# Optimization experiments

Measured on AMD Instinct MI355X. Metric: run time of the kernel, lower is better.

The kernel has to match this reference:

```python
import jax, jax.numpy as jnp
import numpy as np

N_NODES = 75000
N_EDGES = 1200000


def gcn_conv(x, src, dst, W, b, n):
    # linear transform first (PyG GCNConv applies lin before propagate)
    h = x @ W  # [n, out]
    # add self loops
    loop = jnp.arange(n, dtype=src.dtype)
    s = jnp.concatenate([src, loop])
    d = jnp.concatenate([dst, loop])
    # symmetric normalization: deg computed on destination after self-loops
    deg = jnp.zeros((n,), dtype=h.dtype).at[d].add(1.0)
    dinv = jnp.where(deg > 0, jax.lax.rsqrt(deg), 0.0)
    norm = dinv[s] * dinv[d]  # [E+n]
    msgs = h[s] * norm[:, None]  # gather + scale, [E+n, out]
    out = jax.ops.segment_sum(msgs, d, num_segments=n)  # scatter-add
    return out + b


def setup_inputs() -> dict:
    key = jax.random.key(0)
    ks = jax.random.split(key, 6)
    x = jax.random.normal(ks[0], (N_NODES, 64), dtype=jnp.float32)
    edge_index = jax.random.randint(ks[1], (2, N_EDGES), 0, N_NODES, dtype=jnp.int64)
    # Glorot-ish scaled weights
    W1 = jax.random.normal(ks[2], (64, 64), dtype=jnp.float32) * (1.0 / np.sqrt(64))
    b1 = jax.random.normal(ks[3], (64,), dtype=jnp.float32) * 0.01
    W2 = jax.random.normal(ks[4], (64, 16), dtype=jnp.float32) * (1.0 / np.sqrt(64))
    b2 = jax.random.normal(ks[5], (16,), dtype=jnp.float32) * 0.01
    return {"x": x, "edge_index": edge_index, "W1": W1, "b1": b1, "W2": W2, "b2": b2}


def reference(x, edge_index, W1, b1, W2, b2):
    src, dst = edge_index[0], edge_index[1]
    h = gcn_conv(x, src, dst, W1, b1, N_NODES)
    h = jax.nn.relu(h)
    # dropout is identity in eval mode
    out = gcn_conv(h, src, dst, W2, b2, N_NODES)
    return out
```

## Files before the change

### kernel.cpp

```cpp
#include <hip/hip_runtime.h>


#define NBSHIFT 9
#define BUCKET_NODES 512
#define CAP 10240
#define CHA 8192
#define TA 512
#define TB 512
#define MAXNB 160
#define EPT 16

__device__ __forceinline__ unsigned bfpack(float a, float b) {
  unsigned ua = __float_as_uint(a), ub = __float_as_uint(b);
  ua += 0x7fffu + ((ua >> 16) & 1u);
  ub += 0x7fffu + ((ub >> 16) & 1u);
  return (ua >> 16) | (ub & 0xffff0000u);
}

__launch_bounds__(TA)
__global__ void kA_bucket(const int* __restrict__ src, const int* __restrict__ dst,
                          int* __restrict__ bucketCur, int* __restrict__ bucketArr,
                          int NB, int E) {
  __shared__ int stage[CHA];
  __shared__ unsigned char binOf[CHA];
  __shared__ int cnt[MAXNB];
  __shared__ int off[MAXNB];
  __shared__ int gpos[MAXNB];
  __shared__ int cursor[MAXNB];
  __shared__ int scanbuf[256];
  int t = threadIdx.x;
  int e0 = blockIdx.x * CHA;

  for (int i = t; i < NB; i += TA) cnt[i] = 0;
  __syncthreads();
  int dreg[EPT];
  #pragma unroll
  for (int j = 0; j < EPT; j++) {
    int e = e0 + t + j * TA;
    dreg[j] = (e < E) ? dst[e] : -1;
    if (dreg[j] >= 0) atomicAdd(&cnt[dreg[j] >> NBSHIFT], 1);
  }
  __syncthreads();
  if (t < 256) scanbuf[t] = (t < NB) ? cnt[t] : 0;
  __syncthreads();
  for (int o = 1; o < 256; o <<= 1) {
    int add = (t < 256 && t >= o) ? scanbuf[t - o] : 0;
    __syncthreads();
    if (t < 256) scanbuf[t] += add;
    __syncthreads();
  }
  if (t < NB) {
    off[t] = scanbuf[t] - cnt[t];
    cursor[t] = off[t];
    gpos[t] = (cnt[t] > 0) ? atomicAdd(&bucketCur[t], cnt[t]) : 0;
  }
  __syncthreads();
  #pragma unroll
  for (int j = 0; j < EPT; j++) {
    int e = e0 + t + j * TA;
    if (dreg[j] >= 0) {
      int d = dreg[j], s = src[e];
      int b = d >> NBSHIFT;
      int p = atomicAdd(&cursor[b], 1);
      stage[p] = (s << NBSHIFT) | (d & (BUCKET_NODES - 1));
      binOf[p] = (unsigned char)b;
    }
  }
  __syncthreads();
  int total = scanbuf[255];
  for (int i = t; i < total; i += TA) {
    int b = binOf[i];
    int destIdx = gpos[b] + (i - off[b]);
    if (destIdx < CAP) bucketArr[b * CAP + destIdx] = stage[i];
  }
}

__launch_bounds__(TB)
__global__ void kB_fill(const int* __restrict__ bucketArr, const int* __restrict__ bucketCur,
                        int* __restrict__ rp, float* __restrict__ dinv,
                        int* __restrict__ col, int N, int NB) {
  __shared__ int cnts[MAXNB];
  __shared__ int hist[BUCKET_NODES];
  __shared__ int cur[BUCKET_NODES];
  __shared__ int wsum[8], woff[8];
  __shared__ int s_base;
  int b = blockIdx.x;
  int t = threadIdx.x;
  int nE = min(bucketCur[b], CAP);
  int base = b * CAP;

  if (t < NB) cnts[t] = min(bucketCur[t], CAP);
  hist[t] = 0;
  __syncthreads();
  for (int i = t; i < nE; i += TB)
    atomicAdd(&hist[bucketArr[base + i] & (BUCKET_NODES - 1)], 1);
  __syncthreads();
  int myv = hist[t];
  int lane = t & 63, w = t >> 6;
  int incl = myv;
  #pragma unroll
  for (int o = 1; o < 64; o <<= 1) {
    int v = __shfl_up(incl, o);
    if (lane >= o) incl += v;
  }
  if (lane == 63) wsum[w] = incl;
  __syncthreads();
  if (t == 0) {
    int acc = 0;
    for (int i = 0; i < b; i++) acc += cnts[i];
    s_base = acc;
    int a2 = 0;
    #pragma unroll
    for (int i = 0; i < 8; i++) { woff[i] = a2; a2 += wsum[i]; }
    if (b == NB - 1) rp[N] = acc + nE;
  }
  __syncthreads();
  int gexcl = s_base + woff[w] + (incl - myv);
  cur[t] = gexcl;
  int gnode = b * BUCKET_NODES + t;
  if (gnode < N) {
    rp[gnode] = gexcl;
    dinv[gnode] = rsqrtf((float)(myv + 1));
  }
  __syncthreads();
  for (int i = t; i < nE; i += TB) {
    int v = bucketArr[base + i];
    int p = atomicAdd(&cur[v & (BUCKET_NODES - 1)], 1);
    col[p] = v >> NBSHIFT;
  }
}

__launch_bounds__(256)
__global__ void k_gemm64(const float4* __restrict__ X4, const float4* __restrict__ W4,
                         const float* __restrict__ dinv, uint2* __restrict__ outb,
                         int n) {
  __shared__ float4 Xs[64 * 17];
  __shared__ float4 Ws[64 * 16];
  int t = threadIdx.x;
  int base = blockIdx.x * 64;
  {
    int rr = t >> 2, q = t & 3;
    int r = base + rr;
    #pragma unroll
    for (int c = 0; c < 4; c++) {
      float4 v = make_float4(0.f, 0.f, 0.f, 0.f);
      if (r < n) v = X4[r * 16 + q * 4 + c];
      Xs[rr * 17 + q * 4 + c] = v;
      Ws[t + 256 * c] = W4[t + 256 * c];
    }
  }
  __syncthreads();

  int tx = t & 15, ty = t >> 4;
  float4 a0 = make_float4(0.f, 0.f, 0.f, 0.f), a1 = a0, a2 = a0, a3 = a0;
  #pragma unroll
  for (int kb = 0; kb < 16; kb++) {
    float4 x0 = Xs[(ty * 4 + 0) * 17 + kb];
    float4 x1 = Xs[(ty * 4 + 1) * 17 + kb];
    float4 x2 = Xs[(ty * 4 + 2) * 17 + kb];
    float4 x3 = Xs[(ty * 4 + 3) * 17 + kb];
    float4 w0 = Ws[(kb * 4 + 0) * 16 + tx];
    float4 w1 = Ws[(kb * 4 + 1) * 16 + tx];
    float4 w2 = Ws[(kb * 4 + 2) * 16 + tx];
    float4 w3 = Ws[(kb * 4 + 3) * 16 + tx];
    #define FMA4(A, XS) \
      A.x = fmaf(XS.x, w0.x, A.x); A.y = fmaf(XS.x, w0.y, A.y); \
      A.z = fmaf(XS.x, w0.z, A.z); A.w = fmaf(XS.x, w0.w, A.w); \
      A.x = fmaf(XS.y, w1.x, A.x); A.y = fmaf(XS.y, w1.y, A.y); \
      A.z = fmaf(XS.y, w1.z, A.z); A.w = fmaf(XS.y, w1.w, A.w); \
      A.x = fmaf(XS.z, w2.x, A.x); A.y = fmaf(XS.z, w2.y, A.y); \
      A.z = fmaf(XS.z, w2.z, A.z); A.w = fmaf(XS.z, w2.w, A.w); \
      A.x = fmaf(XS.w, w3.x, A.x); A.y = fmaf(XS.w, w3.y, A.y); \
      A.z = fmaf(XS.w, w3.z, A.z); A.w = fmaf(XS.w, w3.w, A.w);
    FMA4(a0, x0) FMA4(a1, x1) FMA4(a2, x2) FMA4(a3, x3)
    #undef FMA4
  }
  #pragma unroll
  for (int i = 0; i < 4; i++) {
    int r = base + ty * 4 + i;
    if (r < n) {
      float s = dinv[r];
      float4 a = (i == 0) ? a0 : (i == 1) ? a1 : (i == 2) ? a2 : a3;
      uint2 pk;
      pk.x = bfpack(a.x * s, a.y * s);
      pk.y = bfpack(a.z * s, a.w * s);
      outb[r * 16 + tx] = pk;
    }
  }
}

__launch_bounds__(256)
__global__ void k_agg64_w2(const uint2* __restrict__ hsb,
                           const int* __restrict__ rp,
                           const int* __restrict__ col,
                           const float* __restrict__ dinv,
                           const float* __restrict__ b1,
                           const float* __restrict__ W2,
                           unsigned* __restrict__ hs2b,
                           int n) {
  int lane = threadIdx.x & 63;
  int c = lane & 15;
  int sub = lane >> 4;
  int node = (blockIdx.x * blockDim.x + threadIdx.x) >> 6;
  if (node >= n) return;

  float4 b14 = ((const float4*)b1)[c];
  float w2r[16];
  #pragma unroll
  for (int i = 0; i < 16; i++) w2r[i] = W2[(sub * 16 + i) * 16 + c];

  int s0 = rp[node], s1 = rp[node + 1];
  int dt = s1 - s0 + 1;
  float ax = 0.f, ay = 0.f, az = 0.f, aw = 0.f;
  int t = sub;
  int i0 = 0, i1 = 0, i2 = 0, i3 = 0;
  if (t < dt)      i0 = (t == 0) ? node : col[s0 + t - 1];
  if (t + 4 < dt)  i1 = col[s0 + t + 3];
  if (t + 8 < dt)  i2 = col[s0 + t + 7];
  if (t + 12 < dt) i3 = col[s0 + t + 11];
  while (t < dt) {
    int c0 = i0, c1 = i1, c2 = i2, c3 = i3;
    bool h1 = (t + 4) < dt, h2 = (t + 8) < dt, h3 = (t + 12) < dt;
    int tn = t + 16;
    if (tn < dt)      i0 = col[s0 + tn - 1];
    if (tn + 4 < dt)  i1 = col[s0 + tn + 3];
    if (tn + 8 < dt)  i2 = col[s0 + tn + 7];
    if (tn + 12 < dt) i3 = col[s0 + tn + 11];
    uint2 u0 = hsb[c0 * 16 + c];
    uint2 u1 = h1 ? hsb[c1 * 16 + c] : make_uint2(0u, 0u);
    uint2 u2 = h2 ? hsb[c2 * 16 + c] : make_uint2(0u, 0u);
    uint2 u3 = h3 ? hsb[c3 * 16 + c] : make_uint2(0u, 0u);
    ax += __uint_as_float(u0.x << 16) + __uint_as_float(u1.x << 16)
        + __uint_as_float(u2.x << 16) + __uint_as_float(u3.x << 16);
    ay += __uint_as_float(u0.x & 0xffff0000u) + __uint_as_float(u1.x & 0xffff0000u)
        + __uint_as_float(u2.x & 0xffff0000u) + __uint_as_float(u3.x & 0xffff0000u);
    az += __uint_as_float(u0.y << 16) + __uint_as_float(u1.y << 16)
        + __uint_as_float(u2.y << 16) + __uint_as_float(u3.y << 16);
    aw += __uint_as_float(u0.y & 0xffff0000u) + __uint_as_float(u1.y & 0xffff0000u)
        + __uint_as_float(u2.y & 0xffff0000u) + __uint_as_float(u3.y & 0xffff0000u);
    t = tn;
  }
  #pragma unroll
  for (int m = 16; m <= 32; m <<= 1) {
    ax += __shfl_xor(ax, m);
    ay += __shfl_xor(ay, m);
    az += __shfl_xor(az, m);
    aw += __shfl_xor(aw, m);
  }
  float dv = dinv[node];
  float hx = fmaxf(ax * dv + b14.x, 0.f);
  float hy = fmaxf(ay * dv + b14.y, 0.f);
  float hz = fmaxf(az * dv + b14.z, 0.f);
  float hw = fmaxf(aw * dv + b14.w, 0.f);

  float part = 0.f;
  #pragma unroll
  for (int i = 0; i < 16; i++) {
    int srcLane = 4 * sub + (i >> 2);
    float h;
    if ((i & 3) == 0)      h = __shfl(hx, srcLane);
    else if ((i & 3) == 1) h = __shfl(hy, srcLane);
    else if ((i & 3) == 2) h = __shfl(hz, srcLane);
    else                   h = __shfl(hw, srcLane);
    part = fmaf(h, w2r[i], part);
  }
  #pragma unroll
  for (int m = 16; m <= 32; m <<= 1) part += __shfl_xor(part, m);
  part *= dv;
  float pnext = __shfl_down(part, 1);
  if (sub == 0 && (c & 1) == 0) {
    hs2b[node * 8 + (c >> 1)] = bfpack(part, pnext);
  }
}

__launch_bounds__(256)
__global__ void k_agg16(const uint2* __restrict__ hs2b,
                        const int* __restrict__ rp,
                        const int* __restrict__ col,
                        const float* __restrict__ dinv,
                        const float* __restrict__ b2,
                        float4* __restrict__ out4,
                        int n) {
  int lane = threadIdx.x & 63;
  int c = lane & 3;
  int sub = lane >> 2;
  int node = (blockIdx.x * blockDim.x + threadIdx.x) >> 6;
  if (node >= n) return;

  int s0 = rp[node], s1 = rp[node + 1];
  int dt = s1 - s0 + 1;
  float ax = 0.f, ay = 0.f, az = 0.f, aw = 0.f;
  int t = sub;
  int i0 = 0, i1 = 0;
  if (t < dt)      i0 = (t == 0) ? node : col[s0 + t - 1];
  if (t + 16 < dt) i1 = col[s0 + t + 15];
  while (t < dt) {
    int c0 = i0, c1 = i1;
    bool h1 = (t + 16) < dt;
    int tn = t + 32;
    if (tn < dt)      i0 = col[s0 + tn - 1];
    if (tn + 16 < dt) i1 = col[s0 + tn + 15];
    uint2 u0 = hs2b[c0 * 4 + c];
    uint2 u1 = h1 ? hs2b[c1 * 4 + c] : make_uint2(0u, 0u);
    ax += __uint_as_float(u0.x << 16) + __uint_as_float(u1.x << 16);
    ay += __uint_as_float(u0.x & 0xffff0000u) + __uint_as_float(u1.x & 0xffff0000u);
    az += __uint_as_float(u0.y << 16) + __uint_as_float(u1.y << 16);
    aw += __uint_as_float(u0.y & 0xffff0000u) + __uint_as_float(u1.y & 0xffff0000u);
    t = tn;
  }
  #pragma unroll
  for (int m = 4; m <= 32; m <<= 1) {
    ax += __shfl_xor(ax, m);
    ay += __shfl_xor(ay, m);
    az += __shfl_xor(az, m);
    aw += __shfl_xor(aw, m);
  }
  if (sub == 0) {
    float dv = dinv[node];
    float4 b24 = ((const float4*)b2)[c];
    float4 o;
    o.x = ax * dv + b24.x;
    o.y = ay * dv + b24.y;
    o.z = az * dv + b24.z;
    o.w = aw * dv + b24.w;
    out4[node * 4 + c] = o;
  }
}

extern "C" void kernel_launch(void* const* d_in, const int* in_sizes, int n_in,
                              void* d_out, int out_size, void* d_ws, size_t ws_size,
                              hipStream_t stream) {
  const float* x  = (const float*)d_in[0];
  const int* edges = (const int*)d_in[1];
  const float* W1 = (const float*)d_in[2];
  const float* b1 = (const float*)d_in[3];
  const float* W2 = (const float*)d_in[4];
  const float* b2 = (const float*)d_in[5];
  float* out = (float*)d_out;

  const int N = in_sizes[0] / 64;
  const int E = in_sizes[1] / 2;
  const int* src = edges;
  const int* dst = edges + E;
  const int NB = (N + BUCKET_NODES - 1) >> NBSHIFT;

  auto align = [](size_t v) { return (v + 255) & ~(size_t)255; };
  char* p = (char*)d_ws;
  float* dinv       = (float*)p; p += align((size_t)N * 4);
  int*   rp         = (int*)p;   p += align((size_t)(N + 1) * 4);
  int*   bucketCur  = (int*)p;   p += align((size_t)MAXNB * 4);
  int*   col        = (int*)p;   p += align((size_t)E * 4);
  float* hs1        = (float*)p; p += align((size_t)N * 64 * 4);
  float* hs2        = (float*)p; p += align((size_t)N * 16 * 4);
  int* bucketArr = (int*)hs1;

  const int nbA = (E + CHA - 1) / CHA;
  const int nbWave = ((size_t)N * 64 + 255) / 256;

  hipMemsetAsync(bucketCur, 0, (size_t)MAXNB * 4, stream);
  kA_bucket<<<nbA, TA, 0, stream>>>(src, dst, bucketCur, bucketArr, NB, E);
  kB_fill  <<<NB, TB, 0, stream>>>(bucketArr, bucketCur, rp, dinv, col, N, NB);

  k_gemm64  <<<(N + 63) / 64, 256, 0, stream>>>((const float4*)x, (const float4*)W1,
                                                dinv, (uint2*)hs1, N);
  k_agg64_w2<<<nbWave, 256, 0, stream>>>((const uint2*)hs1, rp, col, dinv,
                                         b1, W2, (unsigned*)hs2, N);
  k_agg16   <<<nbWave, 256, 0, stream>>>((const uint2*)hs2, rp, col, dinv,
                                         b2, (float4*)out, N);
}
```

Baseline: 128.7 us.

## Split layer-1 aggregation into two column-panel passes for cache locality

The GEMM output is stored as two 32-channel panels, and the fused aggregation plus W2 kernel runs twice, once per panel. The first pass stores a partial W2 product in a scratch buffer and the second adds it before packing. This shrinks the gathered table per pass so random row gathers are more likely to hit in cache. In exchange, the edge list is traversed twice and an extra partial buffer is written and read.

```diff
diff --git a/kernel.cpp b/kernel.cpp
--- a/kernel.cpp
+++ b/kernel.cpp
@@ -175,6 +175,8 @@
     FMA4(a0, x0) FMA4(a1, x1) FMA4(a2, x2) FMA4(a3, x3)
     #undef FMA4
   }
+  int pblk = tx >> 3;
+  int slot = tx & 7;
   #pragma unroll
   for (int i = 0; i < 4; i++) {
     int r = base + ty * 4 + i;
@@ -184,34 +186,40 @@
       uint2 pk;
       pk.x = bfpack(a.x * s, a.y * s);
       pk.y = bfpack(a.z * s, a.w * s);
-      outb[r * 16 + tx] = pk;
+      outb[(size_t)pblk * n * 8 + r * 8 + slot] = pk;
     }
   }
 }
 
+template<int P>
 __launch_bounds__(256)
-__global__ void k_agg64_w2(const uint2* __restrict__ hsb,
-                           const int* __restrict__ rp,
-                           const int* __restrict__ col,
-                           const float* __restrict__ dinv,
-                           const float* __restrict__ b1,
-                           const float* __restrict__ W2,
-                           unsigned* __restrict__ hs2b,
-                           int n) {
+__global__ void k_agg64_w2p(const unsigned* __restrict__ hs1u,
+                            const int* __restrict__ rp,
+                            const int* __restrict__ col,
+                            const float* __restrict__ dinv,
+                            const float* __restrict__ b1,
+                            const float* __restrict__ W2,
+                            float* __restrict__ pbuf,
+                            unsigned* __restrict__ hs2b,
+                            int n) {
   int lane = threadIdx.x & 63;
   int c = lane & 15;
   int sub = lane >> 4;
   int node = (blockIdx.x * blockDim.x + threadIdx.x) >> 6;
   if (node >= n) return;
 
-  float4 b14 = ((const float4*)b1)[c];
   float w2r[16];
   #pragma unroll
-  for (int i = 0; i < 16; i++) w2r[i] = W2[(sub * 16 + i) * 16 + c];
-
+  for (int i = 0; i < 16; i++)
+    w2r[i] = 0.5f * W2[(32 * P + 16 * (sub & 1) + i) * 16 + c];
+  float2 b12 = ((const float2*)b1)[16 * P + c];
+  float pprev = 0.f;
+  if (P == 1 && sub == 0) pprev = pbuf[node * 16 + c];
+
+  const unsigned* tab = hs1u + (size_t)P * n * 16;
   int s0 = rp[node], s1 = rp[node + 1];
   int dt = s1 - s0 + 1;
-  float ax = 0.f, ay = 0.f, az = 0.f, aw = 0.f;
+  float a0 = 0.f, a1 = 0.f;
   int t = sub;
   int i0 = 0, i1 = 0, i2 = 0, i3 = 0;
   if (t < dt)      i0 = (t == 0) ? node : col[s0 + t - 1];
@@ -226,50 +234,42 @@
     if (tn + 4 < dt)  i1 = col[s0 + tn + 3];
     if (tn + 8 < dt)  i2 = col[s0 + tn + 7];
     if (tn + 12 < dt) i3 = col[s0 + tn + 11];
-    uint2 u0 = hsb[c0 * 16 + c];
-    uint2 u1 = h1 ? hsb[c1 * 16 + c] : make_uint2(0u, 0u);
-    uint2 u2 = h2 ? hsb[c2 * 16 + c] : make_uint2(0u, 0u);
-    uint2 u3 = h3 ? hsb[c3 * 16 + c] : make_uint2(0u, 0u);
-    ax += __uint_as_float(u0.x << 16) + __uint_as_float(u1.x << 16)
-        + __uint_as_float(u2.x << 16) + __uint_as_float(u3.x << 16);
-    ay += __uint_as_float(u0.x & 0xffff0000u) + __uint_as_float(u1.x & 0xffff0000u)
-        + __uint_as_float(u2.x & 0xffff0000u) + __uint_as_float(u3.x & 0xffff0000u);
-    az += __uint_as_float(u0.y << 16) + __uint_as_float(u1.y << 16)
-        + __uint_as_float(u2.y << 16) + __uint_as_float(u3.y << 16);
-    aw += __uint_as_float(u0.y & 0xffff0000u) + __uint_as_float(u1.y & 0xffff0000u)
-        + __uint_as_float(u2.y & 0xffff0000u) + __uint_as_float(u3.y & 0xffff0000u);
+    unsigned u0 = tab[c0 * 16 + c];
+    unsigned u1 = h1 ? tab[c1 * 16 + c] : 0u;
+    unsigned u2 = h2 ? tab[c2 * 16 + c] : 0u;
+    unsigned u3 = h3 ? tab[c3 * 16 + c] : 0u;
+    a0 += __uint_as_float(u0 << 16) + __uint_as_float(u1 << 16)
+        + __uint_as_float(u2 << 16) + __uint_as_float(u3 << 16);
+    a1 += __uint_as_float(u0 & 0xffff0000u) + __uint_as_float(u1 & 0xffff0000u)
+        + __uint_as_float(u2 & 0xffff0000u) + __uint_as_float(u3 & 0xffff0000u);
     t = tn;
   }
   #pragma unroll
   for (int m = 16; m <= 32; m <<= 1) {
-    ax += __shfl_xor(ax, m);
-    ay += __shfl_xor(ay, m);
-    az += __shfl_xor(az, m);
-    aw += __shfl_xor(aw, m);
+    a0 += __shfl_xor(a0, m);
+    a1 += __shfl_xor(a1, m);
   }
   float dv = dinv[node];
-  float hx = fmaxf(ax * dv + b14.x, 0.f);
-  float hy = fmaxf(ay * dv + b14.y, 0.f);
-  float hz = fmaxf(az * dv + b14.z, 0.f);
-  float hw = fmaxf(aw * dv + b14.w, 0.f);
+  float h0 = fmaxf(a0 * dv + b12.x, 0.f);
+  float h1v = fmaxf(a1 * dv + b12.y, 0.f);
 
   float part = 0.f;
   #pragma unroll
   for (int i = 0; i < 16; i++) {
-    int srcLane = 4 * sub + (i >> 2);
-    float h;
-    if ((i & 3) == 0)      h = __shfl(hx, srcLane);
-    else if ((i & 3) == 1) h = __shfl(hy, srcLane);
-    else if ((i & 3) == 2) h = __shfl(hz, srcLane);
-    else                   h = __shfl(hw, srcLane);
+    int srcLane = 8 * (sub & 1) + (i >> 1);
+    float h = (i & 1) ? __shfl(h1v, srcLane) : __shfl(h0, srcLane);
     part = fmaf(h, w2r[i], part);
   }
   #pragma unroll
   for (int m = 16; m <= 32; m <<= 1) part += __shfl_xor(part, m);
-  part *= dv;
-  float pnext = __shfl_down(part, 1);
-  if (sub == 0 && (c & 1) == 0) {
-    hs2b[node * 8 + (c >> 1)] = bfpack(part, pnext);
+
+  if (P == 0) {
+    if (sub == 0) pbuf[node * 16 + c] = part;
+  } else {
+    float tot = (part + pprev) * dv;
+    float tnext = __shfl_down(tot, 1);
+    if (sub == 0 && (c & 1) == 0)
+      hs2b[node * 8 + (c >> 1)] = bfpack(tot, tnext);
   }
 }
 
@@ -352,6 +352,7 @@
   int*   col        = (int*)p;   p += align((size_t)E * 4);
   float* hs1        = (float*)p; p += align((size_t)N * 64 * 4);
   float* hs2        = (float*)p; p += align((size_t)N * 16 * 4);
+  float* pbuf       = (float*)p; p += align((size_t)N * 16 * 4);
   int* bucketArr = (int*)hs1;
 
   const int nbA = (E + CHA - 1) / CHA;
@@ -361,10 +362,12 @@
   kA_bucket<<<nbA, TA, 0, stream>>>(src, dst, bucketCur, bucketArr, NB, E);
   kB_fill  <<<NB, TB, 0, stream>>>(bucketArr, bucketCur, rp, dinv, col, N, NB);
 
-  k_gemm64  <<<(N + 63) / 64, 256, 0, stream>>>((const float4*)x, (const float4*)W1,
-                                                dinv, (uint2*)hs1, N);
-  k_agg64_w2<<<nbWave, 256, 0, stream>>>((const uint2*)hs1, rp, col, dinv,
-                                         b1, W2, (unsigned*)hs2, N);
-  k_agg16   <<<nbWave, 256, 0, stream>>>((const uint2*)hs2, rp, col, dinv,
-                                         b2, (float4*)out, N);
-}
+  k_gemm64<<<(N + 63) / 64, 256, 0, stream>>>((const float4*)x, (const float4*)W1,
+                                              dinv, (uint2*)hs1, N);
+  k_agg64_w2p<0><<<nbWave, 256, 0, stream>>>((const unsigned*)hs1, rp, col, dinv,
+                                             b1, W2, pbuf, nullptr, N);
+  k_agg64_w2p<1><<<nbWave, 256, 0, stream>>>((const unsigned*)hs1, rp, col, dinv,
+                                             b1, W2, pbuf, (unsigned*)hs2, N);
+  k_agg16<<<nbWave, 256, 0, stream>>>((const uint2*)hs2, rp, col, dinv,
+                                      b2, (float4*)out, N);
+}
```

New measurement: 155.6 us. 20.9% more time.

## Split layer-2 GEMM from aggregation and pack multiple nodes per wavefront

Applied to the files above, without the earlier changes.

The fused aggregate-then-W2 kernel is split into a pure layer-1 aggregation kernel that writes a bf16 hidden buffer and a separate small GEMM kernel (W2 held in shared memory) producing the scaled layer-2 features. Both aggregation kernels now process several nodes per 64-lane wavefront (2 for the 64-wide layer, 4 for the 16-wide layer) instead of one. With only about 17 edges per node on average, a full wave per node left many lanes idle, so packing nodes should raise lane utilisation and shorten the shuffle reductions. The cost is an extra kernel launch plus a round trip of the bf16 hidden buffer through global memory.

```diff
diff --git a/kernel.cpp b/kernel.cpp
--- a/kernel.cpp
+++ b/kernel.cpp
@@ -16,6 +16,8 @@
   ub += 0x7fffu + ((ub >> 16) & 1u);
   return (ua >> 16) | (ub & 0xffff0000u);
 }
+__device__ __forceinline__ float bflo(unsigned u) { return __uint_as_float(u << 16); }
+__device__ __forceinline__ float bfhi(unsigned u) { return __uint_as_float(u & 0xffff0000u); }
 
 __launch_bounds__(TA)
 __global__ void kA_bucket(const int* __restrict__ src, const int* __restrict__ dst,
@@ -190,86 +192,106 @@
 }
 
 __launch_bounds__(256)
-__global__ void k_agg64_w2(const uint2* __restrict__ hsb,
-                           const int* __restrict__ rp,
-                           const int* __restrict__ col,
-                           const float* __restrict__ dinv,
-                           const float* __restrict__ b1,
-                           const float* __restrict__ W2,
-                           unsigned* __restrict__ hs2b,
-                           int n) {
+__global__ void k_agg64(const uint2* __restrict__ hsb,
+                        const int* __restrict__ rp,
+                        const int* __restrict__ col,
+                        const float* __restrict__ dinv,
+                        const float* __restrict__ b1,
+                        uint2* __restrict__ h1b,
+                        int n) {
   int lane = threadIdx.x & 63;
-  int c = lane & 15;
-  int sub = lane >> 4;
-  int node = (blockIdx.x * blockDim.x + threadIdx.x) >> 6;
+  int hl = lane & 31;
+  int c = hl & 15;
+  int sub = hl >> 4;
+  int node = ((blockIdx.x * blockDim.x + threadIdx.x) >> 6) * 2 + (lane >> 5);
   if (node >= n) return;
 
   float4 b14 = ((const float4*)b1)[c];
-  float w2r[16];
-  #pragma unroll
-  for (int i = 0; i < 16; i++) w2r[i] = W2[(sub * 16 + i) * 16 + c];
-
   int s0 = rp[node], s1 = rp[node + 1];
   int dt = s1 - s0 + 1;
   float ax = 0.f, ay = 0.f, az = 0.f, aw = 0.f;
   int t = sub;
   int i0 = 0, i1 = 0, i2 = 0, i3 = 0;
-  if (t < dt)      i0 = (t == 0) ? node : col[s0 + t - 1];
-  if (t + 4 < dt)  i1 = col[s0 + t + 3];
-  if (t + 8 < dt)  i2 = col[s0 + t + 7];
-  if (t + 12 < dt) i3 = col[s0 + t + 11];
+  if (t < dt)     i0 = (t == 0) ? node : col[s0 + t - 1];
+  if (t + 2 < dt) i1 = col[s0 + t + 1];
+  if (t + 4 < dt) i2 = col[s0 + t + 3];
+  if (t + 6 < dt) i3 = col[s0 + t + 5];
   while (t < dt) {
     int c0 = i0, c1 = i1, c2 = i2, c3 = i3;
-    bool h1 = (t + 4) < dt, h2 = (t + 8) < dt, h3 = (t + 12) < dt;
-    int tn = t + 16;
-    if (tn < dt)      i0 = col[s0 + tn - 1];
-    if (tn + 4 < dt)  i1 = col[s0 + tn + 3];
-    if (tn + 8 < dt)  i2 = col[s0 + tn + 7];
-    if (tn + 12 < dt) i3 = col[s0 + tn + 11];
+    bool h1_ = (t + 2) < dt, h2_ = (t + 4) < dt, h3_ = (t + 6) < dt;
+    int tn = t + 8;
+    if (tn < dt)     i0 = col[s0 + tn - 1];
+    if (tn + 2 < dt) i1 = col[s0 + tn + 1];
+    if (tn + 4 < dt) i2 = col[s0 + tn + 3];
+    if (tn + 6 < dt) i3 = col[s0 + tn + 5];
     uint2 u0 = hsb[c0 * 16 + c];
-    uint2 u1 = h1 ? hsb[c1 * 16 + c] : make_uint2(0u, 0u);
-    uint2 u2 = h2 ? hsb[c2 * 16 + c] : make_uint2(0u, 0u);
-    uint2 u3 = h3 ? hsb[c3 * 16 + c] : make_uint2(0u, 0u);
-    ax += __uint_as_float(u0.x << 16) + __uint_as_float(u1.x << 16)
-        + __uint_as_float(u2.x << 16) + __uint_as_float(u3.x << 16);
-    ay += __uint_as_float(u0.x & 0xffff0000u) + __uint_as_float(u1.x & 0xffff0000u)
-        + __uint_as_float(u2.x & 0xffff0000u) + __uint_as_float(u3.x & 0xffff0000u);
-    az += __uint_as_float(u0.y << 16) + __uint_as_float(u1.y << 16)
-        + __uint_as_float(u2.y << 16) + __uint_as_float(u3.y << 16);
-    aw += __uint_as_float(u0.y & 0xffff0000u) + __uint_as_float(u1.y & 0xffff0000u)
-        + __uint_as_float(u2.y & 0xffff0000u) + __uint_as_float(u3.y & 0xffff0000u);
+    uint2 u1 = h1_ ? hsb[c1 * 16 + c] : make_uint2(0u, 0u);
+    uint2 u2 = h2_ ? hsb[c2 * 16 + c] : make_uint2(0u, 0u);
+    uint2 u3 = h3_ ? hsb[c3 * 16 + c] : make_uint2(0u, 0u);
+    #define ACC(U) \
+      ax += bflo(U.x); ay += bfhi(U.x); az += bflo(U.y); aw += bfhi(U.y);
+    ACC(u0) ACC(u1) ACC(u2) ACC(u3)
+    #undef ACC
     t = tn;
   }
-  #pragma unroll
-  for (int m = 16; m <= 32; m <<= 1) {
-    ax += __shfl_xor(ax, m);
-    ay += __shfl_xor(ay, m);
-    az += __shfl_xor(az, m);
-    aw += __shfl_xor(aw, m);
-  }
-  float dv = dinv[node];
-  float hx = fmaxf(ax * dv + b14.x, 0.f);
-  float hy = fmaxf(ay * dv + b14.y, 0.f);
-  float hz = fmaxf(az * dv + b14.z, 0.f);
-  float hw = fmaxf(aw * dv + b14.w, 0.f);
-
-  float part = 0.f;
-  #pragma unroll
-  for (int i = 0; i < 16; i++) {
-    int srcLane = 4 * sub + (i >> 2);
-    float h;
-    if ((i & 3) == 0)      h = __shfl(hx, srcLane);
-    else if ((i & 3) == 1) h = __shfl(hy, srcLane);
-    else if ((i & 3) == 2) h = __shfl(hz, srcLane);
-    else                   h = __shfl(hw, srcLane);
-    part = fmaf(h, w2r[i], part);
-  }
-  #pragma unroll
-  for (int m = 16; m <= 32; m <<= 1) part += __shfl_xor(part, m);
-  part *= dv;
-  float pnext = __shfl_down(part, 1);
-  if (sub == 0 && (c & 1) == 0) {
-    hs2b[node * 8 + (c >> 1)] = bfpack(part, pnext);
+  ax += __shfl_xor(ax, 16);
+  ay += __shfl_xor(ay, 16);
+  az += __shfl_xor(az, 16);
+  aw += __shfl_xor(aw, 16);
+  if (sub == 0) {
+    float dv = dinv[node];
+    uint2 pk;
+    pk.x = bfpack(fmaxf(ax * dv + b14.x, 0.f), fmaxf(ay * dv + b14.y, 0.f));
+    pk.y = bfpack(fmaxf(az * dv + b14.z, 0.f), fmaxf(aw * dv + b14.w, 0.f));
+    h1b[node * 16 + c] = pk;
+  }
+}
+
+__launch_bounds__(256)
+__global__ void k_gemmB(const uint2* __restrict__ h1b,
+                        const float4* __restrict__ W24,
+                        const float* __restrict__ dinv,
+                        unsigned* __restrict__ hs2b,
+                        int n) {
+  __shared__ float4 Ws[256];
+  int t = threadIdx.x;
+  Ws[t] = W24[t];
+  __syncthreads();
+  int tx = t & 3, ty = t >> 2;
+  int r0 = blockIdx.x * 256 + ty * 4;
+  float4 a0 = make_float4(0.f, 0.f, 0.f, 0.f), a1 = a0, a2 = a0, a3 = a0;
+  #pragma unroll
+  for (int q = 0; q < 16; q++) {
+    uint2 u0 = (r0 + 0 < n) ? h1b[(r0 + 0) * 16 + q] : make_uint2(0u, 0u);
+    uint2 u1 = (r0 + 1 < n) ? h1b[(r0 + 1) * 16 + q] : make_uint2(0u, 0u);
+    uint2 u2 = (r0 + 2 < n) ? h1b[(r0 + 2) * 16 + q] : make_uint2(0u, 0u);
+    uint2 u3 = (r0 + 3 < n) ? h1b[(r0 + 3) * 16 + q] : make_uint2(0u, 0u);
+    #pragma unroll
+    for (int kk = 0; kk < 4; kk++) {
+      float4 w = Ws[(4 * q + kk) * 4 + tx];
+      float v0 = (kk == 0) ? bflo(u0.x) : (kk == 1) ? bfhi(u0.x) : (kk == 2) ? bflo(u0.y) : bfhi(u0.y);
+      float v1 = (kk == 0) ? bflo(u1.x) : (kk == 1) ? bfhi(u1.x) : (kk == 2) ? bflo(u1.y) : bfhi(u1.y);
+      float v2 = (kk == 0) ? bflo(u2.x) : (kk == 1) ? bfhi(u2.x) : (kk == 2) ? bflo(u2.y) : bfhi(u2.y);
+      float v3 = (kk == 0) ? bflo(u3.x) : (kk == 1) ? bfhi(u3.x) : (kk == 2) ? bflo(u3.y) : bfhi(u3.y);
+      a0.x = fmaf(v0, w.x, a0.x); a0.y = fmaf(v0, w.y, a0.y);
+      a0.z = fmaf(v0, w.z, a0.z); a0.w = fmaf(v0, w.w, a0.w);
+      a1.x = fmaf(v1, w.x, a1.x); a1.y = fmaf(v1, w.y, a1.y);
+      a1.z = fmaf(v1, w.z, a1.z); a1.w = fmaf(v1, w.w, a1.w);
+      a2.x = fmaf(v2, w.x, a2.x); a2.y = fmaf(v2, w.y, a2.y);
+      a2.z = fmaf(v2, w.z, a2.z); a2.w = fmaf(v2, w.w, a2.w);
+      a3.x = fmaf(v3, w.x, a3.x); a3.y = fmaf(v3, w.y, a3.y);
+      a3.z = fmaf(v3, w.z, a3.z); a3.w = fmaf(v3, w.w, a3.w);
+    }
+  }
+  #pragma unroll
+  for (int i = 0; i < 4; i++) {
+    int r = r0 + i;
+    if (r < n) {
+      float dv = dinv[r];
+      float4 a = (i == 0) ? a0 : (i == 1) ? a1 : (i == 2) ? a2 : a3;
+      hs2b[r * 8 + 2 * tx]     = bfpack(a.x * dv, a.y * dv);
+      hs2b[r * 8 + 2 * tx + 1] = bfpack(a.z * dv, a.w * dv);
+    }
   }
 }
 
@@ -282,9 +304,10 @@
                         float4* __restrict__ out4,
                         int n) {
   int lane = threadIdx.x & 63;
-  int c = lane & 3;
-  int sub = lane >> 2;
-  int node = (blockIdx.x * blockDim.x + threadIdx.x) >> 6;
+  int hl = lane & 15;
+  int c = hl & 3;
+  int sub = hl >> 2;
+  int node = ((blockIdx.x * blockDim.x + threadIdx.x) >> 6) * 4 + (lane >> 4);
   if (node >= n) return;
 
   int s0 = rp[node], s1 = rp[node + 1];
@@ -292,24 +315,24 @@
   float ax = 0.f, ay = 0.f, az = 0.f, aw = 0.f;
   int t = sub;
   int i0 = 0, i1 = 0;
-  if (t < dt)      i0 = (t == 0) ? node : col[s0 + t - 1];
-  if (t + 16 < dt) i1 = col[s0 + t + 15];
+  if (t < dt)     i0 = (t == 0) ? node : col[s0 + t - 1];
+  if (t + 4 < dt) i1 = col[s0 + t + 3];
   while (t < dt) {
     int c0 = i0, c1 = i1;
-    bool h1 = (t + 16) < dt;
-    int tn = t + 32;
-    if (tn < dt)      i0 = col[s0 + tn - 1];
-    if (tn + 16 < dt) i1 = col[s0 + tn + 15];
+    bool h1_ = (t + 4) < dt;
+    int tn = t + 8;
+    if (tn < dt)     i0 = col[s0 + tn - 1];
+    if (tn + 4 < dt) i1 = col[s0 + tn + 3];
     uint2 u0 = hs2b[c0 * 4 + c];
-    uint2 u1 = h1 ? hs2b[c1 * 4 + c] : make_uint2(0u, 0u);
-    ax += __uint_as_float(u0.x << 16) + __uint_as_float(u1.x << 16);
-    ay += __uint_as_float(u0.x & 0xffff0000u) + __uint_as_float(u1.x & 0xffff0000u);
-    az += __uint_as_float(u0.y << 16) + __uint_as_float(u1.y << 16);
-    aw += __uint_as_float(u0.y & 0xffff0000u) + __uint_as_float(u1.y & 0xffff0000u);
+    uint2 u1 = h1_ ? hs2b[c1 * 4 + c] : make_uint2(0u, 0u);
+    ax += bflo(u0.x) + bflo(u1.x);
+    ay += bfhi(u0.x) + bfhi(u1.x);
+    az += bflo(u0.y) + bflo(u1.y);
+    aw += bfhi(u0.y) + bfhi(u1.y);
     t = tn;
   }
   #pragma unroll
-  for (int m = 4; m <= 32; m <<= 1) {
+  for (int m = 4; m <= 8; m <<= 1) {
     ax += __shfl_xor(ax, m);
     ay += __shfl_xor(ay, m);
     az += __shfl_xor(az, m);
@@ -351,20 +374,25 @@
   int*   bucketCur  = (int*)p;   p += align((size_t)MAXNB * 4);
   int*   col        = (int*)p;   p += align((size_t)E * 4);
   float* hs1        = (float*)p; p += align((size_t)N * 64 * 4);
-  float* hs2        = (float*)p; p += align((size_t)N * 16 * 4);
+  float* h1b        = (float*)p; p += align((size_t)N * 64 * 2);
+  float* hs2        = (float*)p; p += align((size_t)N * 16 * 2);
   int* bucketArr = (int*)hs1;
 
   const int nbA = (E + CHA - 1) / CHA;
-  const int nbWave = ((size_t)N * 64 + 255) / 256;
+  const int nbW2 = (int)((((size_t)(N + 1) / 2) * 64 + 255) / 256);
+  const int nbW4 = (int)((((size_t)(N + 3) / 4) * 64 + 255) / 256);
 
   hipMemsetAsync(bucketCur, 0, (size_t)MAXNB * 4, stream);
   kA_bucket<<<nbA, TA, 0, stream>>>(src, dst, bucketCur, bucketArr, NB, E);
   kB_fill  <<<NB, TB, 0, stream>>>(bucketArr, bucketCur, rp, dinv, col, N, NB);
 
-  k_gemm64  <<<(N + 63) / 64, 256, 0, stream>>>((const float4*)x, (const float4*)W1,
-                                                dinv, (uint2*)hs1, N);
-  k_agg64_w2<<<nbWave, 256, 0, stream>>>((const uint2*)hs1, rp, col, dinv,
-                                         b1, W2, (unsigned*)hs2, N);
-  k_agg16   <<<nbWave, 256, 0, stream>>>((const uint2*)hs2, rp, col, dinv,
-                                         b2, (float4*)out, N);
-}
+  k_gemm64<<<(N + 63) / 64, 256, 0, stream>>>((const float4*)x, (const float4*)W1,
+                                              dinv, (uint2*)hs1, N);
+  k_agg64 <<<nbW2, 256, 0, stream>>>((const uint2*)hs1, rp, col, dinv,
+                                     b1, (uint2*)h1b, N);
+  k_gemmB <<<(N + 255) / 256, 256, 0, stream>>>((const uint2*)h1b,
+                                                (const float4*)W2, dinv,
+                                                (unsigned*)hs2, N);
+  k_agg16 <<<nbW4, 256, 0, stream>>>((const uint2*)hs2, rp, col, dinv,
+                                     b2, (float4*)out, N);
+}
```

Result: faster. 122.8 us (-4.6%).
